# Performance work log

Measured on AMD Instinct MI355X. Metric: run time of the kernel, lower is better.

## Reference

```python
import jax, jax.numpy as jnp
import numpy as np

D_MODEL, N_HEADS, D_C, D_FF, N_EXPERTS, TOP_K = 1024, 16, 128, 2048, 8, 2
HEAD_DIM = D_MODEL // N_HEADS
THETA = 10000.0
RMS_EPS = float(np.finfo(np.float32).eps)  # torch nn.RMSNorm default eps


def rmsnorm(x, w):
    var = jnp.mean(x * x, axis=-1, keepdims=True)
    return x * jax.lax.rsqrt(var + RMS_EPS) * w


def rotate_half(x):
    x1, x2 = jnp.split(x, 2, axis=-1)
    return jnp.concatenate([-x2, x1], axis=-1)


def rope_cos_sin(ts):
    # ts: (B, L) float timestamps -> cos, sin: (B, L, HEAD_DIM)
    freqs = 1.0 / THETA ** (jnp.arange(0, HEAD_DIM, 2, dtype=jnp.float32) / HEAD_DIM)
    t = ts[..., None] * freqs            # (B, L, HEAD_DIM//2)
    emb = jnp.concatenate([t, t], axis=-1)
    return jnp.cos(emb), jnp.sin(emb)


def setup_inputs() -> dict:
    key = jax.random.key(0)
    ks = jax.random.split(key, 16)
    B, L, D = 4, 1024, D_MODEL
    s = 0.02
    inp = {
        "x": jax.random.normal(ks[0], (B, L, D), jnp.float32),
        "timestamps_q": jnp.tile(jnp.arange(L, dtype=jnp.float32), (B, 1)),
        "timestamps_kv": jnp.tile(jnp.arange(L, dtype=jnp.float32), (B, 1)),
        "attn_norm_w": jnp.ones((D,), jnp.float32),
        "ffn_norm_w": jnp.ones((D,), jnp.float32),
        "w_kv_c": jax.random.normal(ks[1], (D_C, D), jnp.float32) * s,
        "w_kc_up": jax.random.normal(ks[2], (D, D_C), jnp.float32) * s,
        "w_vc_up": jax.random.normal(ks[3], (D, D_C), jnp.float32) * s,
        "w_qr": jax.random.normal(ks[4], (D, D), jnp.float32) * s,
        "w_kr": jax.random.normal(ks[5], (D, D), jnp.float32) * s,
        "w_o": jax.random.normal(ks[6], (D, D), jnp.float32) * s,
        "gate_w": jax.random.normal(ks[7], (N_EXPERTS, D), jnp.float32) * s,
        "expert_bias": jnp.zeros((N_EXPERTS,), jnp.float32),
        "w1": jax.random.normal(ks[8], (N_EXPERTS, 2 * D_FF, D), jnp.float32) * s,
        "w2": jax.random.normal(ks[9], (N_EXPERTS, D, 2 * D_FF), jnp.float32) * s,
    }
    return inp


def reference(x, timestamps_q, timestamps_kv, attn_norm_w, ffn_norm_w,
              w_kv_c, w_kc_up, w_vc_up, w_qr, w_kr, w_o,
              gate_w, expert_bias, w1, w2):
    B, L, D = x.shape
    H, hd = N_HEADS, HEAD_DIM
    scale = hd ** -0.5

    # ---- MLA attention (pre-norm) ----
    h = rmsnorm(x, attn_norm_w)
    c_kv = h @ w_kv_c.T                                    # (B,L,d_c)
    k_c = (c_kv @ w_kc_up.T).reshape(B, L, H, hd).transpose(0, 2, 1, 3)
    v_c = (c_kv @ w_vc_up.T).reshape(B, L, H, hd).transpose(0, 2, 1, 3)
    q_r = (h @ w_qr.T).reshape(B, L, H, hd).transpose(0, 2, 1, 3)
    k_r = (h @ w_kr.T).reshape(B, L, H, hd).transpose(0, 2, 1, 3)

    cos_q, _sin_q = rope_cos_sin(timestamps_q)
    cos_k, _sin_k = rope_cos_sin(timestamps_kv)
    cos_q = cos_q[:, None]  # (B,1,L,hd)
    cos_k = cos_k[:, None]
    # Faithful to source: apply_rotary_pos_emb(q, k, cos_q, cos_k) -> sin := cos_k
    q_r = q_r * cos_q + rotate_half(q_r) * cos_k
    k_r = k_r * cos_q + rotate_half(k_r) * cos_k

    qs = q_r * scale
    attn = jnp.einsum("bhqd,bhkd->bhqk", qs, k_c) + jnp.einsum("bhqd,bhkd->bhqk", qs, k_r)
    attn_w = jax.nn.softmax(attn, axis=-1)
    out = jnp.einsum("bhqk,bhkd->bhqd", attn_w, v_c)
    out = out.transpose(0, 2, 1, 3).reshape(B, L, D) @ w_o.T
    x1 = x + out

    # ---- MoE FFN (pre-norm) ----
    hn = rmsnorm(x1, ffn_norm_w).reshape(-1, D)            # (T, D)
    T = hn.shape[0]
    gate_logits = hn @ gate_w.T + expert_bias              # (T, E)
    gate_probs = jax.nn.softmax(gate_logits, axis=-1)
    topk_w, topk_i = jax.lax.top_k(gate_probs, TOP_K)
    topk_w = topk_w / jnp.sum(topk_w, axis=-1, keepdims=True)

    # dense (T, E) routing weights (top-k indices are unique per token)
    wd = jnp.zeros((T, N_EXPERTS), x.dtype).at[jnp.arange(T)[:, None], topk_i].add(topk_w)

    hmid = jax.nn.silu(jnp.einsum("td,ekd->tek", hn, w1))  # (T,E,2*d_ff)
    y = jnp.einsum("tek,edk->ted", hmid, w2)               # (T,E,D)
    moe_out = jnp.einsum("ted,te->td", y, wd).reshape(B, L, D)

    expert_counts = jnp.zeros((N_EXPERTS,), jnp.float32).at[topk_i.ravel()].add(1.0)
    return x1 + moe_out, expert_counts
```

## Files before the change

### kernel.cpp

```cpp
#include <hip/hip_runtime.h>
#include <hip/hip_bf16.h>

typedef __hip_bfloat16 bf16;
typedef __attribute__((ext_vector_type(8))) unsigned short ushort8v;
typedef __bf16 bf16x8 __attribute__((ext_vector_type(8)));
typedef float f32x4 __attribute__((ext_vector_type(4)));

#define NTOK 4096
#define DMODEL 1024
#define NHEADS 16
#define HD 64
#define DC 128
#define DFF2 4096
#define NEXP 8
#define LSEQ 1024
#define NBATCH 4
#define RMS_EPS 1.1920928955078125e-07f

union U8 { ushort8v u; bf16x8 b; };

__device__ __forceinline__ float bf2f(unsigned short u) {
  return __uint_as_float(((unsigned int)u) << 16);
}
__device__ __forceinline__ unsigned short f2bf(float f) {
  unsigned int u = __float_as_uint(f);
  unsigned int r = (u + 0x7FFF + ((u >> 16) & 1)) >> 16;
  return (unsigned short)r;
}
__device__ __forceinline__ void gload_lds16(const unsigned short* g, unsigned short* l) {
  __builtin_amdgcn_global_load_lds(
      (__attribute__((address_space(1))) void*)(const_cast<unsigned short*>(g)),
      (__attribute__((address_space(3))) void*)(l), 16, 0, 0);
}

__global__ __launch_bounds__(256)
void rmsnorm_kernel(const float* __restrict__ x, const float* __restrict__ w,
                    float* __restrict__ o, unsigned short* __restrict__ ob) {
  int t = blockIdx.x;
  int tid = threadIdx.x;
  const float4* xr = (const float4*)(x + (size_t)t * DMODEL);
  float4 v = xr[tid];
  float ss = v.x * v.x + v.y * v.y + v.z * v.z + v.w * v.w;
#pragma unroll
  for (int off = 32; off > 0; off >>= 1) ss += __shfl_xor(ss, off);
  __shared__ float red[4];
  int wid = tid >> 6, lane = tid & 63;
  if (lane == 0) red[wid] = ss;
  __syncthreads();
  float tot = red[0] + red[1] + red[2] + red[3];
  float scale = rsqrtf(tot * (1.0f / DMODEL) + RMS_EPS);
  float4 wv = ((const float4*)w)[tid];
  float4 ov;
  ov.x = v.x * scale * wv.x;
  ov.y = v.y * scale * wv.y;
  ov.z = v.z * scale * wv.z;
  ov.w = v.w * scale * wv.w;
  if (o) ((float4*)(o + (size_t)t * DMODEL))[tid] = ov;
  if (ob) {
    unsigned short* orow = ob + (size_t)t * DMODEL + tid * 4;
    orow[0] = f2bf(ov.x); orow[1] = f2bf(ov.y);
    orow[2] = f2bf(ov.z); orow[3] = f2bf(ov.w);
  }
}

__global__ __launch_bounds__(256)
void cvt_bf16_kernel(const float* __restrict__ in, unsigned short* __restrict__ o, int n8) {
  int stride = gridDim.x * 256;
  for (int i = blockIdx.x * 256 + threadIdx.x; i < n8; i += stride) {
    float4 a = ((const float4*)in)[2 * i];
    float4 b = ((const float4*)in)[2 * i + 1];
    ushort8v u;
    u[0] = f2bf(a.x); u[1] = f2bf(a.y); u[2] = f2bf(a.z); u[3] = f2bf(a.w);
    u[4] = f2bf(b.x); u[5] = f2bf(b.y); u[6] = f2bf(b.z); u[7] = f2bf(b.w);
    *(ushort8v*)(o + (size_t)i * 8) = u;
  }
}

__global__ __launch_bounds__(256)
void gemm_bf16(const unsigned short* __restrict__ Ab, const unsigned short* __restrict__ Wb,
               float* __restrict__ Cf, const float* __restrict__ addend, int N, int K) {
  __shared__ __align__(16) unsigned short As[128 * 64];
  __shared__ __align__(16) unsigned short Bs[128 * 64];
  int row0 = blockIdx.y * 128;
  int col0 = blockIdx.x * 128;
  int tid = threadIdx.x;
  int w = tid >> 6, l = tid & 63;
  int lr = l >> 3;
  int lc = (l & 7) * 8;

  const unsigned short* aSrc[4];
  const unsigned short* bSrc[4];
#pragma unroll
  for (int i = 0; i < 4; ++i) {
    aSrc[i] = Ab + (size_t)(row0 + i * 32 + w * 8 + lr) * K + lc;
    bSrc[i] = Wb + (size_t)(col0 + i * 32 + w * 8 + lr) * K + lc;
  }

  f32x4 acc[4][4] = {};
  int wr = w >> 1, wc = w & 1;
  int ln = l & 15, lq = l >> 4;

  for (int k0 = 0; k0 < K; k0 += 64) {
#pragma unroll
    for (int i = 0; i < 4; ++i) {
      gload_lds16(aSrc[i] + k0, &As[(i * 4 + w) * 512]);
      gload_lds16(bSrc[i] + k0, &Bs[(i * 4 + w) * 512]);
    }
    __syncthreads();
#pragma unroll
    for (int kk = 0; kk < 2; ++kk) {
      bf16x8 af[4], bfr[4];
#pragma unroll
      for (int m = 0; m < 4; ++m)
        af[m] = *(const bf16x8*)&As[(wr * 64 + m * 16 + ln) * 64 + kk * 32 + lq * 8];
#pragma unroll
      for (int n = 0; n < 4; ++n)
        bfr[n] = *(const bf16x8*)&Bs[(wc * 64 + n * 16 + ln) * 64 + kk * 32 + lq * 8];
#pragma unroll
      for (int m = 0; m < 4; ++m)
#pragma unroll
        for (int n = 0; n < 4; ++n)
          acc[m][n] = __builtin_amdgcn_mfma_f32_16x16x32_bf16(af[m], bfr[n], acc[m][n], 0, 0, 0);
    }
    __syncthreads();
  }

#pragma unroll
  for (int m = 0; m < 4; ++m) {
#pragma unroll
    for (int j = 0; j < 4; ++j) {
      int row = row0 + wr * 64 + m * 16 + lq * 4 + j;
      float* crow = Cf + (size_t)row * N + col0 + wc * 64 + ln;
      const float* arow = addend ? addend + (size_t)row * N + col0 + wc * 64 + ln : nullptr;
#pragma unroll
      for (int n = 0; n < 4; ++n) {
        float vv = acc[m][n][j];
        if (addend) vv += arow[n * 16];
        crow[n * 16] = vv;
      }
    }
  }
}

template <int MODE>
__global__ __launch_bounds__(256)
void moe_mfma(const unsigned short* __restrict__ A, const unsigned short* __restrict__ Wb,
              unsigned short* __restrict__ Cout, const int* __restrict__ tok2e,
              const int* __restrict__ ebase, const int* __restrict__ icnt) {
  constexpr int N = (MODE == 0) ? DFF2 : DMODEL;
  constexpr int K = (MODE == 0) ? DMODEL : DFF2;
  __shared__ __align__(16) unsigned short As[128 * 64];
  __shared__ __align__(16) unsigned short Bs[128 * 64];
  int e = blockIdx.z;
  int base = ebase[e];
  int cnt = icnt[e];
  int row0 = blockIdx.y * 128;
  if (row0 >= cnt) return;
  int col0 = blockIdx.x * 128;
  int tid = threadIdx.x;
  int w = tid >> 6, l = tid & 63;
  int lr = l >> 3;
  int lc = (l & 7) * 8;

  const unsigned short* aSrc[4];
  const unsigned short* bSrc[4];
#pragma unroll
  for (int i = 0; i < 4; ++i) {
    int r = row0 + i * 32 + w * 8 + lr;
    r = r < cnt ? r : cnt - 1;
    if (MODE == 0) {
      int tok = tok2e[base + r] >> 1;
      aSrc[i] = A + (size_t)tok * K + lc;
    } else {
      aSrc[i] = A + (size_t)(base + r) * K + lc;
    }
    int nrow = col0 + i * 32 + w * 8 + lr;
    bSrc[i] = Wb + (size_t)e * N * K + (size_t)nrow * K + lc;
  }

  f32x4 acc[4][4] = {};
  int wr = w >> 1, wc = w & 1;
  int ln16 = l & 15, lq = l >> 4;

  for (int k0 = 0; k0 < K; k0 += 64) {
#pragma unroll
    for (int i = 0; i < 4; ++i) {
      gload_lds16(aSrc[i] + k0, &As[(i * 4 + w) * 512]);
      gload_lds16(bSrc[i] + k0, &Bs[(i * 4 + w) * 512]);
    }
    __syncthreads();
#pragma unroll
    for (int kk = 0; kk < 2; ++kk) {
      bf16x8 af[4], bfr[4];
#pragma unroll
      for (int m = 0; m < 4; ++m)
        af[m] = *(const bf16x8*)&As[(wr * 64 + m * 16 + ln16) * 64 + kk * 32 + lq * 8];
#pragma unroll
      for (int n = 0; n < 4; ++n)
        bfr[n] = *(const bf16x8*)&Bs[(wc * 64 + n * 16 + ln16) * 64 + kk * 32 + lq * 8];
#pragma unroll
      for (int m = 0; m < 4; ++m)
#pragma unroll
        for (int n = 0; n < 4; ++n)
          acc[m][n] = __builtin_amdgcn_mfma_f32_16x16x32_bf16(af[m], bfr[n], acc[m][n], 0, 0, 0);
    }
    __syncthreads();
  }

#pragma unroll
  for (int m = 0; m < 4; ++m) {
#pragma unroll
    for (int j = 0; j < 4; ++j) {
      int r = row0 + wr * 64 + m * 16 + lq * 4 + j;
      if (r < cnt) {
        if (MODE == 0) {
          unsigned short* orow = Cout + (size_t)(base + r) * N + col0 + wc * 64 + ln16;
#pragma unroll
          for (int n = 0; n < 4; ++n) {
            float v = acc[m][n][j];
            float s = v / (1.f + __expf(-v));
            orow[n * 16] = f2bf(s);
          }
        } else {
          int t2 = tok2e[base + r];
          unsigned short* orow = Cout + (size_t)t2 * N + col0 + wc * 64 + ln16;
#pragma unroll
          for (int n = 0; n < 4; ++n) orow[n * 16] = f2bf(acc[m][n][j]);
        }
      }
    }
  }
}

__global__ __launch_bounds__(256)
void rope_kernel(float* __restrict__ q, float* __restrict__ k,
                 const float* __restrict__ kc, const float* __restrict__ tsq,
                 const float* __restrict__ tskv) {
  int t = blockIdx.x;
  int tid = threadIdx.x;
  __shared__ float cq[32], ck[32];
  if (tid < 32) {
    float fr = __expf(-(float)(2 * tid) * (1.0f / HD) * 9.210340371976184f);
    cq[tid] = cosf(tsq[t] * fr);
    ck[tid] = cosf(tskv[t] * fr);
  }
  __syncthreads();
  size_t rb = (size_t)t * DMODEL;
  for (int p = tid; p < 512; p += 256) {
    int hh = p >> 5, d = p & 31;
    int c1 = hh * 64 + d, c2 = c1 + 32;
    float cqd = cq[d], ckd = ck[d];
    float q1 = q[rb + c1], q2 = q[rb + c2];
    q[rb + c1] = (q1 * cqd - q2 * ckd) * 0.125f;
    q[rb + c2] = (q2 * cqd + q1 * ckd) * 0.125f;
    float k1 = k[rb + c1], k2 = k[rb + c2];
    k[rb + c1] = (k1 * cqd - k2 * ckd) + kc[rb + c1];
    k[rb + c2] = (k2 * cqd + k1 * ckd) + kc[rb + c2];
  }
}

__global__ __launch_bounds__(256)
void qk_split_kernel(const float* __restrict__ q, const float* __restrict__ k,
                     unsigned short* __restrict__ Qb, unsigned short* __restrict__ Kb) {
  int t = blockIdx.x;
  int b = t >> 10, lrow = t & 1023;
  int tid = threadIdx.x;
  int c = tid * 4;
  int hh = c >> 6, d = c & 63;
  size_t src = (size_t)t * DMODEL + c;
  size_t dst = ((size_t)(b * NHEADS + hh) * LSEQ + lrow) * HD + d;
  float4 qv = *(const float4*)(q + src);
  float4 kv = *(const float4*)(k + src);
  ushort4 u;
  u.x = f2bf(qv.x); u.y = f2bf(qv.y); u.z = f2bf(qv.z); u.w = f2bf(qv.w);
  *(ushort4*)(Qb + dst) = u;
  u.x = f2bf(kv.x); u.y = f2bf(kv.y); u.z = f2bf(kv.z); u.w = f2bf(kv.w);
  *(ushort4*)(Kb + dst) = u;
}

__global__ __launch_bounds__(256)
void v_split_kernel(const float* __restrict__ v, unsigned short* __restrict__ Vt) {
  __shared__ float tile[128][65];
  int bh = blockIdx.x;
  int lt = blockIdx.y;
  int b = bh >> 4, hh = bh & 15;
  int tid = threadIdx.x;
#pragma unroll
  for (int pass = 0; pass < 8; ++pass) {
    int r = pass * 16 + (tid >> 4);
    int dq = (tid & 15) * 4;
    float4 vv = *(const float4*)(v + (size_t)(b * 1024 + lt * 128 + r) * DMODEL + hh * 64 + dq);
    tile[r][dq + 0] = vv.x; tile[r][dq + 1] = vv.y;
    tile[r][dq + 2] = vv.z; tile[r][dq + 3] = vv.w;
  }
  __syncthreads();
  int d = tid >> 2, seg = (tid & 3) * 32;
  size_t obase = ((size_t)bh * HD + d) * LSEQ + lt * 128 + seg;
  for (int i = 0; i < 32; i += 4) {
    ushort4 u;
    u.x = f2bf(tile[seg + i][d]);
    u.y = f2bf(tile[seg + i + 1][d]);
    u.z = f2bf(tile[seg + i + 2][d]);
    u.w = f2bf(tile[seg + i + 3][d]);
    *(ushort4*)(Vt + obase + i) = u;
  }
}

__global__ __launch_bounds__(256, 2)
void attn_mfma(const unsigned short* __restrict__ Qb, const unsigned short* __restrict__ Kb,
               const unsigned short* __restrict__ Vt, unsigned short* __restrict__ ao) {
  __shared__ unsigned int plds[128 * 128];
  int bh = blockIdx.y;
  int qt = blockIdx.x;
  int tid = threadIdx.x;
  int w = tid >> 6, l = tid & 63;
  int ln = l & 15, lq = l >> 4;
  size_t kvbase = (size_t)bh * LSEQ * HD;
  int qrow0 = qt * 128 + w * 32;

  bf16x8 qh[2][2];
#pragma unroll
  for (int mi = 0; mi < 2; ++mi)
#pragma unroll
    for (int ks = 0; ks < 2; ++ks) {
      size_t o = kvbase + (size_t)(qrow0 + mi * 16 + ln) * HD + ks * 32 + lq * 8;
      qh[mi][ks] = *(const bf16x8*)(Qb + o);
    }

  float l_run[2][4] = {};
  f32x4 oacc[2][4] = {};

  for (int kt = 0; kt < 8; ++kt) {
    int k0 = kt * 128;
    f32x4 sacc[2][8] = {};
#pragma unroll
    for (int ni = 0; ni < 8; ++ni) {
      size_t ko = kvbase + (size_t)(k0 + ni * 16 + ln) * HD + lq * 8;
      bf16x8 kh0 = *(const bf16x8*)(Kb + ko);
      bf16x8 kh1 = *(const bf16x8*)(Kb + ko + 32);
#pragma unroll
      for (int mi = 0; mi < 2; ++mi) {
        f32x4 a = sacc[mi][ni];
        a = __builtin_amdgcn_mfma_f32_16x16x32_bf16(qh[mi][0], kh0, a, 0, 0, 0);
        a = __builtin_amdgcn_mfma_f32_16x16x32_bf16(qh[mi][1], kh1, a, 0, 0, 0);
        sacc[mi][ni] = a;
      }
    }
#pragma unroll
    for (int mi = 0; mi < 2; ++mi)
#pragma unroll
      for (int j = 0; j < 4; ++j) {
        float rs = 0.f;
#pragma unroll
        for (int ni = 0; ni < 8; ++ni) {
          float p = __expf(sacc[mi][ni][j]);
          sacc[mi][ni][j] = p;
          rs += p;
        }
        rs += __shfl_xor(rs, 1);
        rs += __shfl_xor(rs, 2);
        rs += __shfl_xor(rs, 4);
        rs += __shfl_xor(rs, 8);
        l_run[mi][j] += rs;
      }
#pragma unroll
    for (int mi = 0; mi < 2; ++mi)
#pragma unroll
      for (int ni = 0; ni < 8; ++ni)
#pragma unroll
        for (int j = 0; j < 4; ++j) {
          int row = w * 32 + mi * 16 + lq * 4 + j;
          int col = ni * 16 + ln;
          unsigned int u = ((unsigned int)f2bf(sacc[mi][ni][j])) << 16;
          plds[row * 128 + (col ^ ((row & 3) << 3))] = u;
        }
    __syncthreads();
#pragma unroll
    for (int ksp = 0; ksp < 4; ++ksp) {
      bf16x8 ph[2];
#pragma unroll
      for (int mi = 0; mi < 2; ++mi) {
        int row = w * 32 + mi * 16 + ln;
        int c0 = ksp * 32 + lq * 8;
        const unsigned int* pp = &plds[row * 128 + (c0 ^ ((row & 3) << 3))];
        uint4 u0 = *(const uint4*)pp;
        uint4 u1 = *(const uint4*)(pp + 4);
        unsigned int uu[8] = {u0.x, u0.y, u0.z, u0.w, u1.x, u1.y, u1.z, u1.w};
        U8 uh;
#pragma unroll
        for (int jj = 0; jj < 8; ++jj) uh.u[jj] = (unsigned short)(uu[jj] >> 16);
        ph[mi] = uh.b;
      }
#pragma unroll
      for (int ni = 0; ni < 4; ++ni) {
        size_t vo = kvbase + (size_t)(ni * 16 + ln) * LSEQ + k0 + ksp * 32 + lq * 8;
        bf16x8 vh = *(const bf16x8*)(Vt + vo);
#pragma unroll
        for (int mi = 0; mi < 2; ++mi)
          oacc[mi][ni] = __builtin_amdgcn_mfma_f32_16x16x32_bf16(ph[mi], vh, oacc[mi][ni], 0, 0, 0);
      }
    }
    __syncthreads();
  }

  int b = bh >> 4, hh = bh & 15;
#pragma unroll
  for (int mi = 0; mi < 2; ++mi) {
    float inv[4];
#pragma unroll
    for (int j = 0; j < 4; ++j) inv[j] = 1.0f / l_run[mi][j];
#pragma unroll
    for (int ni = 0; ni < 4; ++ni)
#pragma unroll
      for (int j = 0; j < 4; ++j) {
        int tok = b * 1024 + qt * 128 + w * 32 + mi * 16 + lq * 4 + j;
        int col = hh * 64 + ni * 16 + ln;
        ao[(size_t)tok * DMODEL + col] = f2bf(oacc[mi][ni][j] * inv[j]);
      }
  }
}

__global__ __launch_bounds__(256)
void gate_kernel(const float* __restrict__ hn, const float* __restrict__ gw,
                 const float* __restrict__ bias, int* __restrict__ ti,
                 float* __restrict__ tw, int* __restrict__ icnt,
                 float* __restrict__ counts_out) {
  int t = blockIdx.x * 4 + (threadIdx.x >> 6);
  int lane = threadIdx.x & 63;
  const float* hrow = hn + (size_t)t * DMODEL;
  float acc[NEXP];
#pragma unroll
  for (int e = 0; e < NEXP; ++e) acc[e] = 0.f;
  for (int d = lane; d < DMODEL; d += 64) {
    float hv = hrow[d];
#pragma unroll
    for (int e = 0; e < NEXP; ++e) acc[e] += hv * gw[e * DMODEL + d];
  }
#pragma unroll
  for (int e = 0; e < NEXP; ++e)
#pragma unroll
    for (int off = 32; off > 0; off >>= 1) acc[e] += __shfl_xor(acc[e], off);
  if (lane == 0) {
    float lg[NEXP], ex[NEXP];
    float mx = -1e30f;
#pragma unroll
    for (int e = 0; e < NEXP; ++e) {
      lg[e] = acc[e] + bias[e];
      mx = fmaxf(mx, lg[e]);
    }
#pragma unroll
    for (int e = 0; e < NEXP; ++e) ex[e] = expf(lg[e] - mx);
    int i0 = 0;
    float p0 = ex[0];
#pragma unroll
    for (int e = 1; e < NEXP; ++e)
      if (ex[e] > p0) { p0 = ex[e]; i0 = e; }
    int i1 = -1;
    float p1 = -1.f;
#pragma unroll
    for (int e = 0; e < NEXP; ++e)
      if (e != i0 && ex[e] > p1) { p1 = ex[e]; i1 = e; }
    float wsum = p0 + p1;
    ti[2 * t] = i0;
    ti[2 * t + 1] = i1;
    tw[2 * t] = p0 / wsum;
    tw[2 * t + 1] = p1 / wsum;
    atomicAdd(&icnt[i0], 1);
    atomicAdd(&icnt[i1], 1);
    atomicAdd(&counts_out[i0], 1.0f);
    atomicAdd(&counts_out[i1], 1.0f);
  }
}

__global__ void init_kernel(float* __restrict__ counts_out, int* __restrict__ icnt,
                            int* __restrict__ cursor) {
  int i = threadIdx.x;
  if (i < NEXP) {
    counts_out[i] = 0.f;
    icnt[i] = 0;
    cursor[i] = 0;
  }
}

__global__ void scan_kernel(const int* __restrict__ icnt, int* __restrict__ ebase) {
  if (threadIdx.x == 0) {
    int s = 0;
    for (int e = 0; e < NEXP; ++e) {
      ebase[e] = s;
      s += icnt[e];
    }
  }
}

__global__ __launch_bounds__(256)
void scatter_kernel(const int* __restrict__ ti, const int* __restrict__ ebase,
                    int* __restrict__ cursor, int* __restrict__ tok2e) {
  int t = blockIdx.x * 256 + threadIdx.x;
#pragma unroll
  for (int s = 0; s < 2; ++s) {
    int e = ti[2 * t + s];
    int pos = atomicAdd(&cursor[e], 1);
    tok2e[ebase[e] + pos] = 2 * t + s;
  }
}

__global__ __launch_bounds__(256)
void combine_kernel(const float* __restrict__ x1, const unsigned short* __restrict__ y,
                    const float* __restrict__ tw, float* __restrict__ out) {
  int idx = blockIdx.x * 256 + threadIdx.x;
  int t = idx >> 8, c = idx & 255;
  float w0 = tw[2 * t], w1 = tw[2 * t + 1];
  float4 a = ((const float4*)x1)[idx];
  const unsigned short* y0 = y + (size_t)(2 * t) * DMODEL + c * 4;
  const unsigned short* y1 = y0 + DMODEL;
  ushort4 u0 = *(const ushort4*)y0;
  ushort4 u1 = *(const ushort4*)y1;
  float4 o;
  o.x = a.x + w0 * bf2f(u0.x) + w1 * bf2f(u1.x);
  o.y = a.y + w0 * bf2f(u0.y) + w1 * bf2f(u1.y);
  o.z = a.z + w0 * bf2f(u0.z) + w1 * bf2f(u1.z);
  o.w = a.w + w0 * bf2f(u0.w) + w1 * bf2f(u1.w);
  ((float4*)out)[idx] = o;
}

extern "C" void kernel_launch(void* const* d_in, const int* in_sizes, int n_in,
                              void* d_out, int out_size, void* d_ws, size_t ws_size,
                              hipStream_t stream) {
  (void)in_sizes; (void)n_in; (void)ws_size;
  const float* x = (const float*)d_in[0];
  const float* tsq = (const float*)d_in[1];
  const float* tskv = (const float*)d_in[2];
  const float* attn_nw = (const float*)d_in[3];
  const float* ffn_nw = (const float*)d_in[4];
  const float* w_kv_c = (const float*)d_in[5];
  const float* w_kc_up = (const float*)d_in[6];
  const float* w_vc_up = (const float*)d_in[7];
  const float* w_qr = (const float*)d_in[8];
  const float* w_kr = (const float*)d_in[9];
  const float* w_o = (const float*)d_in[10];
  const float* gate_w = (const float*)d_in[11];
  const float* expert_bias = (const float*)d_in[12];
  const float* w1 = (const float*)d_in[13];
  const float* w2 = (const float*)d_in[14];

  float* out = (float*)d_out;
  float* counts_out = out + (out_size - NEXP);

  char* ws = (char*)d_ws;
  size_t off = 0;
  auto alloc = [&](size_t bytes) {
    char* p = ws + off;
    off += (bytes + 255) & ~(size_t)255;
    return p;
  };
  float* h   = (float*)alloc((size_t)NTOK * DMODEL * 4);
  float* qb  = (float*)alloc((size_t)NTOK * DMODEL * 4);
  float* kb  = (float*)alloc((size_t)NTOK * DMODEL * 4);
  float* vb  = (float*)alloc((size_t)NTOK * DMODEL * 4);
  float* kcb = (float*)alloc((size_t)NTOK * DMODEL * 4);
  float* ckv = (float*)alloc((size_t)NTOK * DC * 4);
  unsigned short* yb  = (unsigned short*)alloc((size_t)NTOK * 2 * DMODEL * 2);
  unsigned short* hb  = (unsigned short*)alloc((size_t)NTOK * DMODEL * 2);
  unsigned short* hmid = (unsigned short*)alloc((size_t)NTOK * 2 * DFF2 * 2);
  unsigned short* ckvb = (unsigned short*)alloc((size_t)NTOK * DC * 2);
  unsigned short* wbuf = (unsigned short*)alloc((size_t)DMODEL * DMODEL * 2);
  float* tw  = (float*)alloc((size_t)NTOK * 2 * 4);
  int* ti    = (int*)alloc((size_t)NTOK * 2 * 4);
  int* tok2e = (int*)alloc((size_t)NTOK * 2 * 4);
  int* icnt  = (int*)alloc(NEXP * 4);
  int* ebase = (int*)alloc(NEXP * 4);
  int* cursor = (int*)alloc(NEXP * 4);

  unsigned short* Qb = hmid;
  unsigned short* Kb = hmid + (size_t)4 * 1024 * 1024;
  unsigned short* Vt = hmid + (size_t)8 * 1024 * 1024;
  unsigned short* ao = hmid + (size_t)12 * 1024 * 1024;
  unsigned short* wxb = (unsigned short*)qb;

  init_kernel<<<1, 64, 0, stream>>>(counts_out, icnt, cursor);
  rmsnorm_kernel<<<NTOK, 256, 0, stream>>>(x, attn_nw, nullptr, hb);
  cvt_bf16_kernel<<<512, 256, 0, stream>>>(w_qr, wbuf, DMODEL * DMODEL / 8);
  gemm_bf16<<<dim3(8, 32), 256, 0, stream>>>(hb, wbuf, qb, nullptr, DMODEL, DMODEL);
  cvt_bf16_kernel<<<512, 256, 0, stream>>>(w_kr, wbuf, DMODEL * DMODEL / 8);
  gemm_bf16<<<dim3(8, 32), 256, 0, stream>>>(hb, wbuf, kb, nullptr, DMODEL, DMODEL);
  cvt_bf16_kernel<<<64, 256, 0, stream>>>(w_kv_c, wbuf, DC * DMODEL / 8);
  gemm_bf16<<<dim3(1, 32), 256, 0, stream>>>(hb, wbuf, ckv, nullptr, DC, DMODEL);
  cvt_bf16_kernel<<<256, 256, 0, stream>>>(ckv, ckvb, NTOK * DC / 8);
  cvt_bf16_kernel<<<64, 256, 0, stream>>>(w_kc_up, wbuf, DMODEL * DC / 8);
  gemm_bf16<<<dim3(8, 32), 256, 0, stream>>>(ckvb, wbuf, kcb, nullptr, DMODEL, DC);
  cvt_bf16_kernel<<<64, 256, 0, stream>>>(w_vc_up, wbuf, DMODEL * DC / 8);
  gemm_bf16<<<dim3(8, 32), 256, 0, stream>>>(ckvb, wbuf, vb, nullptr, DMODEL, DC);
  rope_kernel<<<NTOK, 256, 0, stream>>>(qb, kb, kcb, tsq, tskv);
  qk_split_kernel<<<NTOK, 256, 0, stream>>>(qb, kb, Qb, Kb);
  v_split_kernel<<<dim3(64, 8), 256, 0, stream>>>(vb, Vt);
  attn_mfma<<<dim3(8, 64), 256, 0, stream>>>(Qb, Kb, Vt, ao);
  cvt_bf16_kernel<<<512, 256, 0, stream>>>(w_o, wbuf, DMODEL * DMODEL / 8);
  gemm_bf16<<<dim3(8, 32), 256, 0, stream>>>(ao, wbuf, h, x, DMODEL, DMODEL);
  rmsnorm_kernel<<<NTOK, 256, 0, stream>>>(h, ffn_nw, qb, hb);
  gate_kernel<<<NTOK / 4, 256, 0, stream>>>(qb, gate_w, expert_bias, ti, tw, icnt, counts_out);
  scan_kernel<<<1, 64, 0, stream>>>(icnt, ebase);
  scatter_kernel<<<NTOK / 256, 256, 0, stream>>>(ti, ebase, cursor, tok2e);
  cvt_bf16_kernel<<<2048, 256, 0, stream>>>(w1, wxb, NEXP * DFF2 * DMODEL / 8);
  moe_mfma<0><<<dim3(DFF2 / 128, NTOK / 128, NEXP), 256, 0, stream>>>(hb, wxb, hmid, tok2e, ebase, icnt);
  cvt_bf16_kernel<<<2048, 256, 0, stream>>>(w2, wxb, NEXP * DMODEL * DFF2 / 8);
  moe_mfma<1><<<dim3(DMODEL / 128, NTOK / 128, NEXP), 256, 0, stream>>>(hmid, wxb, yb, tok2e, ebase, icnt);
  combine_kernel<<<NTOK, 256, 0, stream>>>(h, yb, tw, out);
}
```

Before: 814.9 us.

## Double-buffer MoE expert GEMMs with 256-row tiles and 512-thread blocks

```diff
diff --git a/kernel.cpp b/kernel.cpp
--- a/kernel.cpp
+++ b/kernel.cpp
@@ -143,87 +143,123 @@
 }
 
 template <int MODE>
-__global__ __launch_bounds__(256)
-void moe_mfma(const unsigned short* __restrict__ A, const unsigned short* __restrict__ Wb,
-              unsigned short* __restrict__ Cout, const int* __restrict__ tok2e,
-              const int* __restrict__ ebase, const int* __restrict__ icnt) {
-  constexpr int N = (MODE == 0) ? DFF2 : DMODEL;
-  constexpr int K = (MODE == 0) ? DMODEL : DFF2;
-  __shared__ __align__(16) unsigned short As[128 * 64];
-  __shared__ __align__(16) unsigned short Bs[128 * 64];
+__global__ __launch_bounds__(512)
+void moe_gemm2(const unsigned short* __restrict__ A, const unsigned short* __restrict__ W_,
+               unsigned short* __restrict__ Cb, const int* __restrict__ tok2e,
+               const int* __restrict__ ebase, const int* __restrict__ icnt) {
+  constexpr int N = (MODE == 2) ? DFF2 : DMODEL;
+  constexpr int K = (MODE == 2) ? DMODEL : DFF2;
+  __shared__ __align__(16) unsigned short As[2][256 * 64];
+  __shared__ __align__(16) unsigned short Bs[2][128 * 64];
   int e = blockIdx.z;
   int base = ebase[e];
   int cnt = icnt[e];
-  int row0 = blockIdx.y * 128;
+  int row0 = blockIdx.y * 256;
   if (row0 >= cnt) return;
   int col0 = blockIdx.x * 128;
   int tid = threadIdx.x;
   int w = tid >> 6, l = tid & 63;
-  int lr = l >> 3;
-  int lc = (l & 7) * 8;
-
-  const unsigned short* aSrc[4];
-  const unsigned short* bSrc[4];
-#pragma unroll
-  for (int i = 0; i < 4; ++i) {
-    int r = row0 + i * 32 + w * 8 + lr;
+  int lr = l >> 3, lc = (l & 7) * 8;
+
+  const unsigned short* aP[4];
+  const unsigned short* bP[2];
+#pragma unroll
+  for (int p = 0; p < 4; ++p) {
+    int r = row0 + p * 64 + w * 8 + lr;
     r = r < cnt ? r : cnt - 1;
-    if (MODE == 0) {
-      int tok = tok2e[base + r] >> 1;
-      aSrc[i] = A + (size_t)tok * K + lc;
-    } else {
-      aSrc[i] = A + (size_t)(base + r) * K + lc;
-    }
-    int nrow = col0 + i * 32 + w * 8 + lr;
-    bSrc[i] = Wb + (size_t)e * N * K + (size_t)nrow * K + lc;
-  }
+    if (MODE == 2)
+      aP[p] = A + (size_t)(tok2e[base + r] >> 1) * K + lc;
+    else
+      aP[p] = A + (size_t)(base + r) * K + lc;
+  }
+  const unsigned short* Wp = W_ + (size_t)e * N * K;
+#pragma unroll
+  for (int p = 0; p < 2; ++p)
+    bP[p] = Wp + (size_t)(col0 + p * 64 + w * 8 + lr) * K + lc;
 
   f32x4 acc[4][4] = {};
-  int wr = w >> 1, wc = w & 1;
-  int ln16 = l & 15, lq = l >> 4;
-
-  for (int k0 = 0; k0 < K; k0 += 64) {
-#pragma unroll
-    for (int i = 0; i < 4; ++i) {
-      gload_lds16(aSrc[i] + k0, &As[(i * 4 + w) * 512]);
-      gload_lds16(bSrc[i] + k0, &Bs[(i * 4 + w) * 512]);
+  int wm = w >> 1, wn = w & 1;
+  int ln = l & 15, lq = l >> 4;
+
+  constexpr int NT = K >> 6;
+  {
+    unsigned short* ab = &As[0][0];
+    unsigned short* bb = &Bs[0][0];
+#pragma unroll
+    for (int p = 0; p < 4; ++p) gload_lds16(aP[p], ab + (p * 64 + w * 8) * 64);
+#pragma unroll
+    for (int p = 0; p < 2; ++p) gload_lds16(bP[p], bb + (p * 64 + w * 8) * 64);
+  }
+  __syncthreads();
+  int cur = 0;
+  for (int t = 0; t < NT - 1; ++t) {
+    {
+      unsigned short* ab = &As[cur ^ 1][0];
+      unsigned short* bb = &Bs[cur ^ 1][0];
+      int k0 = (t + 1) << 6;
+#pragma unroll
+      for (int p = 0; p < 4; ++p) gload_lds16(aP[p] + k0, ab + (p * 64 + w * 8) * 64);
+#pragma unroll
+      for (int p = 0; p < 2; ++p) gload_lds16(bP[p] + k0, bb + (p * 64 + w * 8) * 64);
+    }
+    {
+      const unsigned short* ab = &As[cur][0];
+      const unsigned short* bb = &Bs[cur][0];
+#pragma unroll
+      for (int kk = 0; kk < 2; ++kk) {
+        bf16x8 af[4], bfr[4];
+#pragma unroll
+        for (int m = 0; m < 4; ++m)
+          af[m] = *(const bf16x8*)&ab[(wm * 64 + m * 16 + ln) * 64 + kk * 32 + lq * 8];
+#pragma unroll
+        for (int n = 0; n < 4; ++n)
+          bfr[n] = *(const bf16x8*)&bb[(wn * 64 + n * 16 + ln) * 64 + kk * 32 + lq * 8];
+#pragma unroll
+        for (int m = 0; m < 4; ++m)
+#pragma unroll
+          for (int n = 0; n < 4; ++n)
+            acc[m][n] = __builtin_amdgcn_mfma_f32_16x16x32_bf16(af[m], bfr[n], acc[m][n], 0, 0, 0);
+      }
     }
     __syncthreads();
+    cur ^= 1;
+  }
+  {
+    const unsigned short* ab = &As[cur][0];
+    const unsigned short* bb = &Bs[cur][0];
 #pragma unroll
     for (int kk = 0; kk < 2; ++kk) {
       bf16x8 af[4], bfr[4];
 #pragma unroll
       for (int m = 0; m < 4; ++m)
-        af[m] = *(const bf16x8*)&As[(wr * 64 + m * 16 + ln16) * 64 + kk * 32 + lq * 8];
+        af[m] = *(const bf16x8*)&ab[(wm * 64 + m * 16 + ln) * 64 + kk * 32 + lq * 8];
 #pragma unroll
       for (int n = 0; n < 4; ++n)
-        bfr[n] = *(const bf16x8*)&Bs[(wc * 64 + n * 16 + ln16) * 64 + kk * 32 + lq * 8];
+        bfr[n] = *(const bf16x8*)&bb[(wn * 64 + n * 16 + ln) * 64 + kk * 32 + lq * 8];
 #pragma unroll
       for (int m = 0; m < 4; ++m)
 #pragma unroll
         for (int n = 0; n < 4; ++n)
           acc[m][n] = __builtin_amdgcn_mfma_f32_16x16x32_bf16(af[m], bfr[n], acc[m][n], 0, 0, 0);
     }
-    __syncthreads();
   }
 
 #pragma unroll
   for (int m = 0; m < 4; ++m) {
 #pragma unroll
     for (int j = 0; j < 4; ++j) {
-      int r = row0 + wr * 64 + m * 16 + lq * 4 + j;
+      int r = row0 + wm * 64 + m * 16 + lq * 4 + j;
       if (r < cnt) {
-        if (MODE == 0) {
-          unsigned short* orow = Cout + (size_t)(base + r) * N + col0 + wc * 64 + ln16;
+        if (MODE == 2) {
+          unsigned short* orow = Cb + (size_t)(base + r) * N + col0 + wn * 64 + ln;
 #pragma unroll
           for (int n = 0; n < 4; ++n) {
             float v = acc[m][n][j];
-            float s = v / (1.f + __expf(-v));
-            orow[n * 16] = f2bf(s);
+            orow[n * 16] = f2bf(v / (1.f + __expf(-v)));
           }
         } else {
           int t2 = tok2e[base + r];
-          unsigned short* orow = Cout + (size_t)t2 * N + col0 + wc * 64 + ln16;
+          unsigned short* orow = Cb + (size_t)t2 * N + col0 + wn * 64 + ln;
 #pragma unroll
           for (int n = 0; n < 4; ++n) orow[n * 16] = f2bf(acc[m][n][j]);
         }
@@ -601,8 +637,8 @@
   scan_kernel<<<1, 64, 0, stream>>>(icnt, ebase);
   scatter_kernel<<<NTOK / 256, 256, 0, stream>>>(ti, ebase, cursor, tok2e);
   cvt_bf16_kernel<<<2048, 256, 0, stream>>>(w1, wxb, NEXP * DFF2 * DMODEL / 8);
-  moe_mfma<0><<<dim3(DFF2 / 128, NTOK / 128, NEXP), 256, 0, stream>>>(hb, wxb, hmid, tok2e, ebase, icnt);
+  moe_gemm2<2><<<dim3(DFF2 / 128, NTOK / 256, NEXP), 512, 0, stream>>>(hb, wxb, hmid, tok2e, ebase, icnt);
   cvt_bf16_kernel<<<2048, 256, 0, stream>>>(w2, wxb, NEXP * DMODEL * DFF2 / 8);
-  moe_mfma<1><<<dim3(DMODEL / 128, NTOK / 128, NEXP), 256, 0, stream>>>(hmid, wxb, yb, tok2e, ebase, icnt);
+  moe_gemm2<3><<<dim3(DMODEL / 128, NTOK / 256, NEXP), 512, 0, stream>>>(hmid, wxb, yb, tok2e, ebase, icnt);
   combine_kernel<<<NTOK, 256, 0, stream>>>(h, yb, tw, out);
 }
```

New measurement: 919.0 us. 12.8% more time.

## Fuse attention projection GEMMs into concatenated-weight launches and swizzle MoE tile order

Applied to the files above, without the earlier changes.

```diff
diff --git a/kernel.cpp b/kernel.cpp
--- a/kernel.cpp
+++ b/kernel.cpp
@@ -142,6 +142,73 @@
   }
 }
 
+__global__ __launch_bounds__(256)
+void gemm_proj(const unsigned short* __restrict__ Ab, const unsigned short* __restrict__ Wcat,
+               float* __restrict__ d0, float* __restrict__ d1, float* __restrict__ d2,
+               int c1, int c2, int s0, int s1, int s2, int K) {
+  __shared__ __align__(16) unsigned short As[128 * 64];
+  __shared__ __align__(16) unsigned short Bs[128 * 64];
+  int row0 = blockIdx.y * 128;
+  int col0 = blockIdx.x * 128;
+  int tid = threadIdx.x;
+  int w = tid >> 6, l = tid & 63;
+  int lr = l >> 3;
+  int lc = (l & 7) * 8;
+
+  const unsigned short* aSrc[4];
+  const unsigned short* bSrc[4];
+#pragma unroll
+  for (int i = 0; i < 4; ++i) {
+    aSrc[i] = Ab + (size_t)(row0 + i * 32 + w * 8 + lr) * K + lc;
+    bSrc[i] = Wcat + (size_t)(col0 + i * 32 + w * 8 + lr) * K + lc;
+  }
+
+  f32x4 acc[4][4] = {};
+  int wr = w >> 1, wc = w & 1;
+  int ln = l & 15, lq = l >> 4;
+
+  for (int k0 = 0; k0 < K; k0 += 64) {
+#pragma unroll
+    for (int i = 0; i < 4; ++i) {
+      gload_lds16(aSrc[i] + k0, &As[(i * 4 + w) * 512]);
+      gload_lds16(bSrc[i] + k0, &Bs[(i * 4 + w) * 512]);
+    }
+    __syncthreads();
+#pragma unroll
+    for (int kk = 0; kk < 2; ++kk) {
+      bf16x8 af[4], bfr[4];
+#pragma unroll
+      for (int m = 0; m < 4; ++m)
+        af[m] = *(const bf16x8*)&As[(wr * 64 + m * 16 + ln) * 64 + kk * 32 + lq * 8];
+#pragma unroll
+      for (int n = 0; n < 4; ++n)
+        bfr[n] = *(const bf16x8*)&Bs[(wc * 64 + n * 16 + ln) * 64 + kk * 32 + lq * 8];
+#pragma unroll
+      for (int m = 0; m < 4; ++m)
+#pragma unroll
+        for (int n = 0; n < 4; ++n)
+          acc[m][n] = __builtin_amdgcn_mfma_f32_16x16x32_bf16(af[m], bfr[n], acc[m][n], 0, 0, 0);
+    }
+    __syncthreads();
+  }
+
+  float* dst;
+  int cb, stride;
+  if (col0 < c1) { dst = d0; cb = 0; stride = s0; }
+  else if (col0 < c2) { dst = d1; cb = c1; stride = s1; }
+  else { dst = d2; cb = c2; stride = s2; }
+#pragma unroll
+  for (int m = 0; m < 4; ++m) {
+#pragma unroll
+    for (int j = 0; j < 4; ++j) {
+      int row = row0 + wr * 64 + m * 16 + lq * 4 + j;
+      float* crow = dst + (size_t)row * stride + (col0 - cb) + wc * 64 + ln;
+#pragma unroll
+      for (int n = 0; n < 4; ++n) crow[n * 16] = acc[m][n][j];
+    }
+  }
+}
+
 template <int MODE>
 __global__ __launch_bounds__(256)
 void moe_mfma(const unsigned short* __restrict__ A, const unsigned short* __restrict__ Wb,
@@ -154,9 +221,18 @@
   int e = blockIdx.z;
   int base = ebase[e];
   int cnt = icnt[e];
-  int row0 = blockIdx.y * 128;
+  int bx = blockIdx.x, by = blockIdx.y;
+  if (MODE == 0) {
+    int nx = gridDim.x, ny = gridDim.y;
+    int T = nx * ny;
+    int lin = bx + nx * by;
+    int nl = (lin & 7) * (T >> 3) + (lin >> 3);
+    by = nl & (ny - 1);
+    bx = nl / ny;
+  }
+  int row0 = by * 128;
   if (row0 >= cnt) return;
-  int col0 = blockIdx.x * 128;
+  int col0 = bx * 128;
   int tid = threadIdx.x;
   int w = tid >> 6, l = tid & 63;
   int lr = l >> 3;
@@ -563,7 +639,7 @@
   unsigned short* hb  = (unsigned short*)alloc((size_t)NTOK * DMODEL * 2);
   unsigned short* hmid = (unsigned short*)alloc((size_t)NTOK * 2 * DFF2 * 2);
   unsigned short* ckvb = (unsigned short*)alloc((size_t)NTOK * DC * 2);
-  unsigned short* wbuf = (unsigned short*)alloc((size_t)DMODEL * DMODEL * 2);
+  unsigned short* wbuf = (unsigned short*)alloc((size_t)2176 * DMODEL * 2);
   float* tw  = (float*)alloc((size_t)NTOK * 2 * 4);
   int* ti    = (int*)alloc((size_t)NTOK * 2 * 4);
   int* tok2e = (int*)alloc((size_t)NTOK * 2 * 4);
@@ -580,16 +656,15 @@
   init_kernel<<<1, 64, 0, stream>>>(counts_out, icnt, cursor);
   rmsnorm_kernel<<<NTOK, 256, 0, stream>>>(x, attn_nw, nullptr, hb);
   cvt_bf16_kernel<<<512, 256, 0, stream>>>(w_qr, wbuf, DMODEL * DMODEL / 8);
-  gemm_bf16<<<dim3(8, 32), 256, 0, stream>>>(hb, wbuf, qb, nullptr, DMODEL, DMODEL);
-  cvt_bf16_kernel<<<512, 256, 0, stream>>>(w_kr, wbuf, DMODEL * DMODEL / 8);
-  gemm_bf16<<<dim3(8, 32), 256, 0, stream>>>(hb, wbuf, kb, nullptr, DMODEL, DMODEL);
-  cvt_bf16_kernel<<<64, 256, 0, stream>>>(w_kv_c, wbuf, DC * DMODEL / 8);
-  gemm_bf16<<<dim3(1, 32), 256, 0, stream>>>(hb, wbuf, ckv, nullptr, DC, DMODEL);
+  cvt_bf16_kernel<<<512, 256, 0, stream>>>(w_kr, wbuf + (size_t)1024 * DMODEL, DMODEL * DMODEL / 8);
+  cvt_bf16_kernel<<<64, 256, 0, stream>>>(w_kv_c, wbuf + (size_t)2048 * DMODEL, DC * DMODEL / 8);
+  gemm_proj<<<dim3(17, 32), 256, 0, stream>>>(hb, wbuf, qb, kb, ckv,
+                                              1024, 2048, DMODEL, DMODEL, DC, DMODEL);
   cvt_bf16_kernel<<<256, 256, 0, stream>>>(ckv, ckvb, NTOK * DC / 8);
   cvt_bf16_kernel<<<64, 256, 0, stream>>>(w_kc_up, wbuf, DMODEL * DC / 8);
-  gemm_bf16<<<dim3(8, 32), 256, 0, stream>>>(ckvb, wbuf, kcb, nullptr, DMODEL, DC);
-  cvt_bf16_kernel<<<64, 256, 0, stream>>>(w_vc_up, wbuf, DMODEL * DC / 8);
-  gemm_bf16<<<dim3(8, 32), 256, 0, stream>>>(ckvb, wbuf, vb, nullptr, DMODEL, DC);
+  cvt_bf16_kernel<<<64, 256, 0, stream>>>(w_vc_up, wbuf + (size_t)1024 * DC, DMODEL * DC / 8);
+  gemm_proj<<<dim3(16, 32), 256, 0, stream>>>(ckvb, wbuf, kcb, vb, vb,
+                                              1024, 2048, DMODEL, DMODEL, DMODEL, DC);
   rope_kernel<<<NTOK, 256, 0, stream>>>(qb, kb, kcb, tsq, tskv);
   qk_split_kernel<<<NTOK, 256, 0, stream>>>(qb, kb, Qb, Kb);
   v_split_kernel<<<dim3(64, 8), 256, 0, stream>>>(vb, Vt);
```

Result: no change. 801.0 us (-1.7%).
